# Optimization experiments

Hardware: AMD Instinct MI355X
Metric: run time of the kernel (lower is better)

## Reference

```python
import jax, jax.numpy as jnp
import numpy as np

B, S, A, H, NH = 4, 4096, 512, 1024, 16
HD = H // NH  # 64


def setup_inputs() -> dict:
    key = jax.random.key(0)
    ks = jax.random.split(key, 12)
    s = 1.0 / np.sqrt(H)
    return {
        "hidden_states": jax.random.normal(ks[0], (B, S, H), jnp.float32),
        "audio_tokens": jax.random.normal(ks[1], (B, A, H), jnp.float32),
        "attention_mask": jax.random.randint(ks[2], (B, A), 0, 2, jnp.int32),
        "Wq": jax.random.normal(ks[3], (H, H), jnp.float32) * s,
        "bq": jnp.zeros((H,), jnp.float32),
        "Wk": jax.random.normal(ks[4], (H, H), jnp.float32) * s,
        "bk": jnp.zeros((H,), jnp.float32),
        "Wv": jax.random.normal(ks[5], (H, H), jnp.float32) * s,
        "bv": jnp.zeros((H,), jnp.float32),
        "Wo": jax.random.normal(ks[6], (H, H), jnp.float32) * s,
        "bo": jnp.zeros((H,), jnp.float32),
        "ln_gamma": jnp.ones((H,), jnp.float32),
        "ln_beta": jnp.zeros((H,), jnp.float32),
        "residual_scale": jnp.asarray(0.05, jnp.float32),
    }


def _san(x, big=10000.0):
    return jnp.nan_to_num(x, nan=0.0, posinf=big, neginf=-big)


def reference(hidden_states, audio_tokens, attention_mask, Wq, bq, Wk, bk, Wv, bv,
              Wo, bo, ln_gamma, ln_beta, residual_scale):
    hs = _san(hidden_states).astype(jnp.float32)
    at = _san(audio_tokens).astype(jnp.float32)

    def heads(x, W, b):  # [b, t, H] -> [b, t, nh, hd]
        return _san(x @ W.T + b).reshape(x.shape[0], x.shape[1], NH, HD)

    q = heads(hs, Wq, bq)            # [B,S,NH,HD]
    k = heads(at, Wk, bk)            # [B,A,NH,HD]
    v = heads(at, Wv, bv)            # [B,A,NH,HD]

    scale = max(np.sqrt(HD), 1e-8)
    scores = jnp.einsum("bsnd,band->bnsa", q, k) / scale  # [B,NH,S,A]
    scores = jnp.clip(_san(jnp.clip(scores, -50.0, 50.0), 50.0), -50.0, 50.0)

    attend = (attention_mask > 0)[:, None, None, :]       # [B,1,1,A]
    scores = jnp.where(attend, scores, -10000.0)
    scores = jnp.clip(scores, -50.0, 50.0)

    probs = jax.nn.softmax(scores, axis=-1)
    probs = _san(probs, 1.0)
    probs = probs / (jnp.sum(probs, axis=-1, keepdims=True) + 1e-8)

    ctx = jnp.einsum("bnsa,band->bsnd", probs, v).reshape(B, S, H)
    delta = _san(ctx @ Wo.T + bo)

    rs = jnp.clip(residual_scale, 0.0, 0.3)
    delta = rs * delta

    mu = jnp.mean(delta, axis=-1, keepdims=True)
    var = jnp.mean(jnp.square(delta - mu), axis=-1, keepdims=True)
    delta = (delta - mu) / jnp.sqrt(var + 1e-5) * ln_gamma + ln_beta
    return delta
```

## Files before the change

### kernel.cpp

```cpp
#include <hip/hip_runtime.h>
#include <hip/hip_bf16.h>
#include <cstdint>
#include <cstddef>

#define B_  4
#define S_  4096
#define A_  512
#define H_  1024
#define NH_ 16
#define HD_ 64

typedef __bf16 bf16;
typedef __bf16 bf16x8 __attribute__((ext_vector_type(8)));
typedef __bf16 bf16x4 __attribute__((ext_vector_type(4)));
typedef float  fx4    __attribute__((ext_vector_type(4)));

typedef __attribute__((address_space(3))) void LDS_v;
typedef const __attribute__((address_space(1))) void GLB_v;

__device__ __forceinline__ void gl_lds16(const void* g, void* l) {
    __builtin_amdgcn_global_load_lds((GLB_v*)g, (LDS_v*)l, 16, 0, 0);
}

__device__ __forceinline__ float sanf(float x) {
    if (x != x) return 0.f;
    if (fabsf(x) == __builtin_inff()) return x > 0.f ? 10000.f : -10000.f;
    return x;
}

__global__ __launch_bounds__(256) void cast_all(const float* __restrict__ hs,
                                                const float* __restrict__ at,
                                                const float* __restrict__ wq,
                                                const float* __restrict__ wk,
                                                const float* __restrict__ wv,
                                                const float* __restrict__ wo,
                                                bf16* __restrict__ dhs, bf16* __restrict__ dat,
                                                bf16* __restrict__ dwq, bf16* __restrict__ dwk,
                                                bf16* __restrict__ dwv, bf16* __restrict__ dwo) {
    int i = blockIdx.x * 256 + threadIdx.x;
    const float* s; bf16* d; int off;
    if (i < 4194304)      { s = hs; d = dhs; off = i; }
    else if (i < 4718592) { s = at; d = dat; off = i - 4194304; }
    else if (i < 4980736) { s = wq; d = dwq; off = i - 4718592; }
    else if (i < 5242880) { s = wk; d = dwk; off = i - 4980736; }
    else if (i < 5505024) { s = wv; d = dwv; off = i - 5242880; }
    else                  { s = wo; d = dwo; off = i - 5505024; }
    float4 v = ((const float4*)s)[off];
    bf16x4 o;
    o[0] = (bf16)sanf(v.x); o[1] = (bf16)sanf(v.y);
    o[2] = (bf16)sanf(v.z); o[3] = (bf16)sanf(v.w);
    *(bf16x4*)&d[(size_t)off * 4] = o;
}

__global__ __launch_bounds__(256) void qkv_gemm(const bf16* __restrict__ hsb,
                                                const bf16* __restrict__ atb,
                                                const bf16* __restrict__ wqb,
                                                const bf16* __restrict__ wkb,
                                                const bf16* __restrict__ wvb,
                                                const float* __restrict__ bq,
                                                const float* __restrict__ bk,
                                                const float* __restrict__ bv,
                                                bf16* __restrict__ Qb,
                                                bf16* __restrict__ Kb,
                                                bf16* __restrict__ Vtb) {
    __shared__ __align__(16) bf16 As[128 * 32];
    __shared__ __align__(16) bf16 Bs[128 * 32];

    const int id = blockIdx.x;
    int mode, m0, n0;
    const bf16 *A, *Bt; const float* bias;
    if (id < 1024)      { mode = 0; m0 = (id & 127) * 128; n0 = (id >> 7) * 128; A = hsb; Bt = wqb; bias = bq; }
    else if (id < 1152) { int t = id - 1024; mode = 1; m0 = (t & 15) * 128; n0 = (t >> 4) * 128; A = atb; Bt = wkb; bias = bk; }
    else                { int t = id - 1152; mode = 2; m0 = (t & 15) * 128; n0 = (t >> 4) * 128; A = atb; Bt = wvb; bias = bv; }

    const int tid  = threadIdx.x;
    const int lane = tid & 63;
    const int wv   = tid >> 6;
    const int wr   = wv >> 1, wc = wv & 1;
    const int lr   = lane & 15, kq = lane >> 4;

    fx4 acc[4][4] = {};

    const bf16* Ag = A  + (size_t)m0 * 1024;
    const bf16* Bg = Bt + (size_t)n0 * 1024;
    const int c0 = tid, c1 = tid + 256;
    const int row0 = c0 >> 2, kc0 = c0 & 3;
    const int row1 = c1 >> 2, kc1 = c1 & 3;

    for (int k0 = 0; k0 < 1024; k0 += 32) {
        gl_lds16(Ag + (size_t)row0 * 1024 + k0 + kc0 * 8, &As[c0 * 8]);
        gl_lds16(Ag + (size_t)row1 * 1024 + k0 + kc1 * 8, &As[c1 * 8]);
        gl_lds16(Bg + (size_t)row0 * 1024 + k0 + kc0 * 8, &Bs[c0 * 8]);
        gl_lds16(Bg + (size_t)row1 * 1024 + k0 + kc1 * 8, &Bs[c1 * 8]);
        __syncthreads();
        bf16x8 af[4], bfr[4];
#pragma unroll
        for (int i = 0; i < 4; i++) af[i]  = *(const bf16x8*)&As[(wr * 64 + i * 16 + lr) * 32 + kq * 8];
#pragma unroll
        for (int j = 0; j < 4; j++) bfr[j] = *(const bf16x8*)&Bs[(wc * 64 + j * 16 + lr) * 32 + kq * 8];
#pragma unroll
        for (int i = 0; i < 4; i++)
#pragma unroll
            for (int j = 0; j < 4; j++)
                acc[i][j] = __builtin_amdgcn_mfma_f32_16x16x32_bf16(af[i], bfr[j], acc[i][j], 0, 0, 0);
        __syncthreads();
    }

    float bb[4];
#pragma unroll
    for (int j = 0; j < 4; j++) bb[j] = bias[n0 + wc * 64 + j * 16 + lr];

    if (mode == 0) {
        const float sc = 0.18033688011112042f;
#pragma unroll
        for (int i = 0; i < 4; i++) {
            int row = m0 + wr * 64 + i * 16 + kq * 4;
#pragma unroll
            for (int j = 0; j < 4; j++) {
                int col = n0 + wc * 64 + j * 16 + lr;
#pragma unroll
                for (int r = 0; r < 4; r++)
                    Qb[(size_t)(row + r) * 1024 + col] = (bf16)((acc[i][j][r] + bb[j]) * sc);
            }
        }
    } else if (mode == 1) {
#pragma unroll
        for (int i = 0; i < 4; i++) {
            int row = m0 + wr * 64 + i * 16 + kq * 4;
#pragma unroll
            for (int j = 0; j < 4; j++) {
                int col = n0 + wc * 64 + j * 16 + lr;
#pragma unroll
                for (int r = 0; r < 4; r++)
                    Kb[(size_t)(row + r) * 1024 + col] = (bf16)(acc[i][j][r] + bb[j]);
            }
        }
    } else {
#pragma unroll
        for (int i = 0; i < 4; i++) {
            int m = m0 + wr * 64 + i * 16 + kq * 4;
            int bidx = m >> 9, a = m & 511;
#pragma unroll
            for (int j = 0; j < 4; j++) {
                int col = n0 + wc * 64 + j * 16 + lr;
                bf16x4 o;
#pragma unroll
                for (int r = 0; r < 4; r++) o[r] = (bf16)(acc[i][j][r] + bb[j]);
                *(bf16x4*)&Vtb[((size_t)bidx * H_ + col) * A_ + a] = o;
            }
        }
    }
}

__global__ __launch_bounds__(256) void gemm_o(const bf16* __restrict__ A,
                                              const bf16* __restrict__ Bt,
                                              const float* __restrict__ bias,
                                              bf16* __restrict__ C,
                                              const float* __restrict__ rsp) {
    __shared__ __align__(16) bf16 As[128 * 32];
    __shared__ __align__(16) bf16 Bs[128 * 32];

    const int tid  = threadIdx.x;
    const int lane = tid & 63;
    const int wv   = tid >> 6;
    const int wr   = wv >> 1, wc = wv & 1;
    const int lr   = lane & 15, kq = lane >> 4;
    const int m0   = blockIdx.x * 128, n0 = blockIdx.y * 128;

    fx4 acc[4][4] = {};

    const bf16* Ag = A  + (size_t)m0 * 1024;
    const bf16* Bg = Bt + (size_t)n0 * 1024;
    const int c0 = tid, c1 = tid + 256;
    const int row0 = c0 >> 2, kc0 = c0 & 3;
    const int row1 = c1 >> 2, kc1 = c1 & 3;

    for (int k0 = 0; k0 < 1024; k0 += 32) {
        gl_lds16(Ag + (size_t)row0 * 1024 + k0 + kc0 * 8, &As[c0 * 8]);
        gl_lds16(Ag + (size_t)row1 * 1024 + k0 + kc1 * 8, &As[c1 * 8]);
        gl_lds16(Bg + (size_t)row0 * 1024 + k0 + kc0 * 8, &Bs[c0 * 8]);
        gl_lds16(Bg + (size_t)row1 * 1024 + k0 + kc1 * 8, &Bs[c1 * 8]);
        __syncthreads();
        bf16x8 af[4], bfr[4];
#pragma unroll
        for (int i = 0; i < 4; i++) af[i]  = *(const bf16x8*)&As[(wr * 64 + i * 16 + lr) * 32 + kq * 8];
#pragma unroll
        for (int j = 0; j < 4; j++) bfr[j] = *(const bf16x8*)&Bs[(wc * 64 + j * 16 + lr) * 32 + kq * 8];
#pragma unroll
        for (int i = 0; i < 4; i++)
#pragma unroll
            for (int j = 0; j < 4; j++)
                acc[i][j] = __builtin_amdgcn_mfma_f32_16x16x32_bf16(af[i], bfr[j], acc[i][j], 0, 0, 0);
        __syncthreads();
    }

    float bb[4];
#pragma unroll
    for (int j = 0; j < 4; j++) bb[j] = bias[n0 + wc * 64 + j * 16 + lr];
    float rs = fminf(fmaxf(rsp[0], 0.f), 0.3f);
#pragma unroll
    for (int i = 0; i < 4; i++) {
        int row = m0 + wr * 64 + i * 16 + kq * 4;
#pragma unroll
        for (int j = 0; j < 4; j++) {
            int col = n0 + wc * 64 + j * 16 + lr;
#pragma unroll
            for (int r = 0; r < 4; r++)
                C[(size_t)(row + r) * 1024 + col] = (bf16)(rs * (acc[i][j][r] + bb[j]));
        }
    }
}

__global__ __launch_bounds__(256, 4) void attn_kernel(const bf16* __restrict__ Q,
                                                      const bf16* __restrict__ Kb,
                                                      const bf16* __restrict__ Vt,
                                                      const int* __restrict__ mask,
                                                      bf16* __restrict__ ctx) {
    __shared__ __align__(16) bf16 Qs[128 * 72];
    __shared__ __align__(16) bf16 Ks[64 * 72];
    __shared__ __align__(16) bf16 Vts[64 * 72];
    __shared__ float smask[512];

    const int tid  = threadIdx.x;
    const int lane = tid & 63;
    const int wv   = tid >> 6;
    const int lr   = lane & 15, kq = lane >> 4;
    const int st = blockIdx.x, h = blockIdx.y, b = blockIdx.z;
    const int m0 = b * S_ + st * 128;
    const float LO = -72.134752f;

    bf16x8 qtmp[4];
#pragma unroll
    for (int i = 0; i < 4; i++) {
        int c = tid + i * 256, row = c >> 3, ch = c & 7;
        qtmp[i] = *(const bf16x8*)(Q + (size_t)(m0 + row) * H_ + h * 64 + ch * 8);
    }
    smask[tid]       = (mask[b * A_ + tid] > 0)       ? -LO : LO;
    smask[tid + 256] = (mask[b * A_ + tid + 256] > 0) ? -LO : LO;
#pragma unroll
    for (int i = 0; i < 4; i++) {
        int c = tid + i * 256, row = c >> 3, ch = c & 7;
        *(bf16x8*)&Qs[row * 72 + ch * 8] = qtmp[i];
    }

    const int srow = tid >> 2, sseg = tid & 3;
    const size_t kg = (size_t)(b * A_ + srow) * H_ + h * 64 + sseg * 16;
    const bf16* vrow = Vt + (size_t)(b * H_ + h * 64 + srow) * A_;
    const int va0 = 32 * (sseg >> 1) + 4 * ((2 * sseg) & 3);
    const int va1 = 32 * (sseg >> 1) + 4 * ((2 * sseg + 1) & 3);

    bf16x8 kr0 = *(const bf16x8*)(Kb + kg);
    bf16x8 kr1 = *(const bf16x8*)(Kb + kg + 8);
    bf16x4 v00 = *(const bf16x4*)(vrow + va0);
    bf16x4 v01 = *(const bf16x4*)(vrow + va0 + 16);
    bf16x4 v10 = *(const bf16x4*)(vrow + va1);
    bf16x4 v11 = *(const bf16x4*)(vrow + va1 + 16);

    fx4 acco[2][4] = {};
    fx4 accd[2] = {};

    bf16x8 vone;
#pragma unroll
    for (int e = 0; e < 8; e++) vone[e] = (bf16)1.0f;

    for (int it = 0; it < 8; it++) {
        const int a0 = it * 64;
        __syncthreads();
        *(bf16x8*)&Ks[srow * 72 + sseg * 16]      = kr0;
        *(bf16x8*)&Ks[srow * 72 + sseg * 16 + 8]  = kr1;
        *(bf16x8*)&Vts[srow * 72 + sseg * 16] =
            __builtin_shufflevector(v00, v01, 0, 1, 2, 3, 4, 5, 6, 7);
        *(bf16x8*)&Vts[srow * 72 + sseg * 16 + 8] =
            __builtin_shufflevector(v10, v11, 0, 1, 2, 3, 4, 5, 6, 7);
        __syncthreads();

        if (it < 7) {
            const size_t ko = kg + (size_t)(a0 + 64) * H_;
            kr0 = *(const bf16x8*)(Kb + ko);
            kr1 = *(const bf16x8*)(Kb + ko + 8);
            v00 = *(const bf16x4*)(vrow + a0 + 64 + va0);
            v01 = *(const bf16x4*)(vrow + a0 + 64 + va0 + 16);
            v10 = *(const bf16x4*)(vrow + a0 + 64 + va1);
            v11 = *(const bf16x4*)(vrow + a0 + 64 + va1 + 16);
        }

        fx4 accs[4][2] = {};
#pragma unroll
        for (int kk = 0; kk < 64; kk += 32) {
            bf16x8 kf[4], qf[2];
#pragma unroll
            for (int mt = 0; mt < 4; mt++)
                kf[mt] = *(const bf16x8*)&Ks[(mt * 16 + lr) * 72 + kk + kq * 8];
#pragma unroll
            for (int nt = 0; nt < 2; nt++)
                qf[nt] = *(const bf16x8*)&Qs[(wv * 32 + nt * 16 + lr) * 72 + kk + kq * 8];
#pragma unroll
            for (int mt = 0; mt < 4; mt++)
#pragma unroll
                for (int nt = 0; nt < 2; nt++)
                    accs[mt][nt] = __builtin_amdgcn_mfma_f32_16x16x32_bf16(kf[mt], qf[nt], accs[mt][nt], 0, 0, 0);
        }

        bf16x8 pa[2][2];
#pragma unroll
        for (int mt = 0; mt < 4; mt++) {
            fx4 cap = *(const fx4*)&smask[a0 + mt * 16 + kq * 4];
#pragma unroll
            for (int nt = 0; nt < 2; nt++) {
#pragma unroll
                for (int r = 0; r < 4; r++) {
                    float p = __builtin_amdgcn_exp2f(fminf(accs[mt][nt][r], cap[r]));
                    pa[mt >> 1][nt][(mt & 1) * 4 + r] = (bf16)p;
                }
            }
        }

#pragma unroll
        for (int ks = 0; ks < 2; ks++) {
#pragma unroll
            for (int stl = 0; stl < 2; stl++)
                accd[stl] = __builtin_amdgcn_mfma_f32_16x16x32_bf16(pa[ks][stl], vone, accd[stl], 0, 0, 0);
#pragma unroll
            for (int dt = 0; dt < 4; dt++) {
                bf16x8 vf = *(const bf16x8*)&Vts[(dt * 16 + lr) * 72 + ks * 32 + kq * 8];
#pragma unroll
                for (int stl = 0; stl < 2; stl++)
                    acco[stl][dt] = __builtin_amdgcn_mfma_f32_16x16x32_bf16(pa[ks][stl], vf, acco[stl][dt], 0, 0, 0);
            }
        }
    }

#pragma unroll
    for (int stl = 0; stl < 2; stl++) {
        float ri[4];
#pragma unroll
        for (int r = 0; r < 4; r++) ri[r] = __builtin_amdgcn_rcpf(accd[stl][r]);
#pragma unroll
        for (int dt = 0; dt < 4; dt++)
#pragma unroll
            for (int r = 0; r < 4; r++)
                Qs[(wv * 32 + stl * 16 + kq * 4 + r) * 72 + dt * 16 + lr] =
                    (bf16)(acco[stl][dt][r] * ri[r]);
    }
    __syncthreads();
#pragma unroll
    for (int i = 0; i < 4; i++) {
        int c = tid + i * 256, row = c >> 3, ch = c & 7;
        *(bf16x8*)&ctx[(size_t)(m0 + row) * H_ + h * 64 + ch * 8] = *(const bf16x8*)&Qs[row * 72 + ch * 8];
    }
}

__global__ __launch_bounds__(256) void ln_kernel(const bf16* __restrict__ in,
                                                 float* __restrict__ out,
                                                 const float* __restrict__ gamma,
                                                 const float* __restrict__ beta) {
    __shared__ float red[8];
    const int tid = threadIdx.x;
    bf16x4 xb = *(const bf16x4*)&in[(size_t)blockIdx.x * 1024 + tid * 4];
    float x0 = (float)xb[0], x1 = (float)xb[1], x2 = (float)xb[2], x3 = (float)xb[3];
    float s = x0 + x1 + x2 + x3;
    float q = x0 * x0 + x1 * x1 + x2 * x2 + x3 * x3;
#pragma unroll
    for (int off = 32; off > 0; off >>= 1) {
        s += __shfl_down(s, off);
        q += __shfl_down(q, off);
    }
    if ((tid & 63) == 0) { red[(tid >> 6) * 2] = s; red[(tid >> 6) * 2 + 1] = q; }
    __syncthreads();
    s = red[0] + red[2] + red[4] + red[6];
    q = red[1] + red[3] + red[5] + red[7];
    float mean = s * (1.f / 1024.f);
    float var  = q * (1.f / 1024.f) - mean * mean;
    float inv  = rsqrtf(var + 1e-5f);
    float4 g  = ((const float4*)gamma)[tid];
    float4 bb = ((const float4*)beta)[tid];
    float4 y;
    y.x = (x0 - mean) * inv * g.x + bb.x;
    y.y = (x1 - mean) * inv * g.y + bb.y;
    y.z = (x2 - mean) * inv * g.z + bb.z;
    y.w = (x3 - mean) * inv * g.w + bb.w;
    ((float4*)(out + (size_t)blockIdx.x * 1024))[tid] = y;
}

extern "C" void kernel_launch(void* const* d_in, const int* in_sizes, int n_in,
                              void* d_out, int out_size, void* d_ws, size_t ws_size,
                              hipStream_t stream) {
    const float* hs    = (const float*)d_in[0];
    const float* at    = (const float*)d_in[1];
    const int*   maskp = (const int*)d_in[2];
    const float* Wq    = (const float*)d_in[3];
    const float* bq    = (const float*)d_in[4];
    const float* Wk    = (const float*)d_in[5];
    const float* bk    = (const float*)d_in[6];
    const float* Wv    = (const float*)d_in[7];
    const float* bv    = (const float*)d_in[8];
    const float* Wo    = (const float*)d_in[9];
    const float* bo    = (const float*)d_in[10];
    const float* gamma = (const float*)d_in[11];
    const float* beta  = (const float*)d_in[12];
    const float* rsp   = (const float*)d_in[13];

    char* ws = (char*)d_ws;
    bf16* hsb = (bf16*)(ws + 0);
    bf16* ctx = (bf16*)(ws + 0);
    bf16* atb = (bf16*)(ws + 33554432);
    bf16* wqb = (bf16*)(ws + 37748736);
    bf16* wkb = (bf16*)(ws + 39845888);
    bf16* wvb = (bf16*)(ws + 41943040);
    bf16* wob = (bf16*)(ws + 44040192);
    bf16* Qb  = (bf16*)(ws + 46137344);
    bf16* Ob  = Qb;
    bf16* Kb  = (bf16*)(ws + 79691776);
    bf16* Vtb = (bf16*)(ws + 83886080);

    cast_all<<<22528, 256, 0, stream>>>(hs, at, Wq, Wk, Wv, Wo,
                                        hsb, atb, wqb, wkb, wvb, wob);

    qkv_gemm<<<1280, 256, 0, stream>>>(hsb, atb, wqb, wkb, wvb,
                                       bq, bk, bv, Qb, Kb, Vtb);

    attn_kernel<<<dim3(32, 16, 4), 256, 0, stream>>>(Qb, Kb, Vtb, maskp, ctx);

    gemm_o<<<dim3(128, 8), 256, 0, stream>>>(ctx, wob, bo, Ob, rsp);
    ln_kernel<<<16384, 256, 0, stream>>>(Ob, (float*)d_out, gamma, beta);
}
```

Measured before the change: 322.6 us.

## Use double-buffered 256x256 GEMM kernel for Q and output projections

Replaces the simple 128x128 single-buffered GEMMs used for the Q projection and the output projection with a new 512-thread 256x256-tile kernel. It double-buffers LDS, prefetches the next K slice during the MFMA phases, applies an XOR swizzle to LDS reads, raises wave priority around MFMA bursts and remaps block IDs for locality. The K/V projections are split into their own smaller kernel. The goal is to hide global-load latency and raise MFMA utilisation on the two large GEMMs. The cost is heavy register use from 8x4 accumulators per wave and only 256 blocks per launch, which may leave compute units underfilled.

```diff
diff --git a/kernel.cpp b/kernel.cpp
--- a/kernel.cpp
+++ b/kernel.cpp
@@ -52,26 +52,196 @@
     *(bf16x4*)&d[(size_t)off * 4] = o;
 }
 
-__global__ __launch_bounds__(256) void qkv_gemm(const bf16* __restrict__ hsb,
-                                                const bf16* __restrict__ atb,
-                                                const bf16* __restrict__ wqb,
-                                                const bf16* __restrict__ wkb,
-                                                const bf16* __restrict__ wvb,
-                                                const float* __restrict__ bq,
-                                                const float* __restrict__ bk,
-                                                const float* __restrict__ bv,
-                                                bf16* __restrict__ Qb,
-                                                bf16* __restrict__ Kb,
-                                                bf16* __restrict__ Vtb) {
+__global__ __launch_bounds__(512, 2) void gemm256(const bf16* __restrict__ A,
+                                                  const bf16* __restrict__ Bt,
+                                                  const float* __restrict__ bias,
+                                                  bf16* __restrict__ C,
+                                                  const int emode,
+                                                  const float* __restrict__ rsp) {
+    __shared__ __align__(16) bf16 lds[2][2][2][256][32];
+
+    const int tid  = threadIdx.x;
+    const int lane = tid & 63;
+    const int w8   = tid >> 6;
+    const int wm   = w8 >> 2, wn = w8 & 3;
+    const int lr   = lane & 15, kq = lane >> 4;
+    const int swz  = ((lr >> 3) & 1) << 4;
+
+    const int sid = ((blockIdx.x & 7) << 5) | (blockIdx.x >> 3);
+    const int m0 = (sid & 63) << 8, n0 = (sid >> 6) << 8;
+
+    const int g = lane ^ (((lane >> 5) & 1) << 1);
+    const bf16* Asrc = A  + (size_t)(m0 + w8 * 32 + (g >> 2)) * 1024 + (g & 3) * 8;
+    const bf16* Bsrc = Bt + (size_t)(n0 + w8 * 32 + (g >> 2)) * 1024 + (g & 3) * 8;
+
+#define STG(MS_, kh_, kt_, si_) do {                                                   \
+        const bf16* s_ = (MS_ ? Bsrc : Asrc) + (kt_) * 64 + (kh_) * 32;                \
+        gl_lds16(s_,                 &lds[si_][MS_][kh_][w8 * 32][0]      + lane * 8); \
+        gl_lds16(s_ + (size_t)16384, &lds[si_][MS_][kh_][w8 * 32 + 16][0] + lane * 8); \
+    } while (0)
+
+#define DSRA(i_, ks_, bi_) (*(const bf16x8*)(&lds[bi_][0][ks_][0][0] + \
+        ((((wm * 128 + (i_) * 16 + lr) * 32 + kq * 8)) ^ swz)))
+#define DSRB(j_, ks_, bi_) (*(const bf16x8*)(&lds[bi_][1][ks_][0][0] + \
+        ((((wn * 64 + (j_) * 16 + lr) * 32 + kq * 8)) ^ swz)))
+
+    fx4 acc[8][4] = {};
+
+    STG(0, 0, 0, 0); STG(1, 0, 0, 0); STG(0, 1, 0, 0); STG(1, 1, 0, 0);
+    asm volatile("s_waitcnt vmcnt(4)" ::: "memory");
+    __builtin_amdgcn_s_barrier();
+
+    for (int kt = 0; kt < 15; ++kt) {
+        const int bi = kt & 1, si = bi ^ 1, kn = kt + 1;
+        bf16x8 af[4], bfr[4];
+
+#pragma unroll
+        for (int j = 0; j < 4; j++) bfr[j] = DSRB(j, 0, bi);
+#pragma unroll
+        for (int i = 0; i < 4; i++) af[i] = DSRA(i, 0, bi);
+        STG(0, 0, kn, si);
+        __builtin_amdgcn_s_barrier();
+        asm volatile("s_waitcnt lgkmcnt(0)" ::: "memory");
+        __builtin_amdgcn_s_setprio(1);
+#pragma unroll
+        for (int i = 0; i < 4; i++)
+#pragma unroll
+            for (int j = 0; j < 4; j++)
+                acc[i][j] = __builtin_amdgcn_mfma_f32_16x16x32_bf16(af[i], bfr[j], acc[i][j], 0, 0, 0);
+        __builtin_amdgcn_s_setprio(0);
+        __builtin_amdgcn_s_barrier();
+
+#pragma unroll
+        for (int i = 0; i < 4; i++) af[i] = DSRA(i + 4, 0, bi);
+        STG(1, 0, kn, si);
+        __builtin_amdgcn_s_barrier();
+        asm volatile("s_waitcnt lgkmcnt(0)" ::: "memory");
+        __builtin_amdgcn_s_setprio(1);
+#pragma unroll
+        for (int i = 0; i < 4; i++)
+#pragma unroll
+            for (int j = 0; j < 4; j++)
+                acc[i + 4][j] = __builtin_amdgcn_mfma_f32_16x16x32_bf16(af[i], bfr[j], acc[i + 4][j], 0, 0, 0);
+        __builtin_amdgcn_s_setprio(0);
+        asm volatile("s_waitcnt vmcnt(4)" ::: "memory");
+        __builtin_amdgcn_s_barrier();
+
+#pragma unroll
+        for (int j = 0; j < 4; j++) bfr[j] = DSRB(j, 1, bi);
+#pragma unroll
+        for (int i = 0; i < 4; i++) af[i] = DSRA(i, 1, bi);
+        STG(0, 1, kn, si);
+        __builtin_amdgcn_s_barrier();
+        asm volatile("s_waitcnt lgkmcnt(0)" ::: "memory");
+        __builtin_amdgcn_s_setprio(1);
+#pragma unroll
+        for (int i = 0; i < 4; i++)
+#pragma unroll
+            for (int j = 0; j < 4; j++)
+                acc[i][j] = __builtin_amdgcn_mfma_f32_16x16x32_bf16(af[i], bfr[j], acc[i][j], 0, 0, 0);
+        __builtin_amdgcn_s_setprio(0);
+        __builtin_amdgcn_s_barrier();
+
+#pragma unroll
+        for (int i = 0; i < 4; i++) af[i] = DSRA(i + 4, 1, bi);
+        STG(1, 1, kn, si);
+        __builtin_amdgcn_s_barrier();
+        asm volatile("s_waitcnt lgkmcnt(0)" ::: "memory");
+        __builtin_amdgcn_s_setprio(1);
+#pragma unroll
+        for (int i = 0; i < 4; i++)
+#pragma unroll
+            for (int j = 0; j < 4; j++)
+                acc[i + 4][j] = __builtin_amdgcn_mfma_f32_16x16x32_bf16(af[i], bfr[j], acc[i + 4][j], 0, 0, 0);
+        __builtin_amdgcn_s_setprio(0);
+        asm volatile("s_waitcnt vmcnt(4)" ::: "memory");
+        __builtin_amdgcn_s_barrier();
+    }
+
+    {
+        const int bi = 1;
+        bf16x8 af[4], bfr[4];
+#pragma unroll
+        for (int j = 0; j < 4; j++) bfr[j] = DSRB(j, 0, bi);
+#pragma unroll
+        for (int i = 0; i < 4; i++) af[i] = DSRA(i, 0, bi);
+        __builtin_amdgcn_s_setprio(1);
+#pragma unroll
+        for (int i = 0; i < 4; i++)
+#pragma unroll
+            for (int j = 0; j < 4; j++)
+                acc[i][j] = __builtin_amdgcn_mfma_f32_16x16x32_bf16(af[i], bfr[j], acc[i][j], 0, 0, 0);
+        __builtin_amdgcn_s_setprio(0);
+#pragma unroll
+        for (int i = 0; i < 4; i++) af[i] = DSRA(i + 4, 0, bi);
+        __builtin_amdgcn_s_setprio(1);
+#pragma unroll
+        for (int i = 0; i < 4; i++)
+#pragma unroll
+            for (int j = 0; j < 4; j++)
+                acc[i + 4][j] = __builtin_amdgcn_mfma_f32_16x16x32_bf16(af[i], bfr[j], acc[i + 4][j], 0, 0, 0);
+        __builtin_amdgcn_s_setprio(0);
+        asm volatile("s_waitcnt vmcnt(0)" ::: "memory");
+        __builtin_amdgcn_s_barrier();
+#pragma unroll
+        for (int j = 0; j < 4; j++) bfr[j] = DSRB(j, 1, bi);
+#pragma unroll
+        for (int i = 0; i < 4; i++) af[i] = DSRA(i, 1, bi);
+        __builtin_amdgcn_s_setprio(1);
+#pragma unroll
+        for (int i = 0; i < 4; i++)
+#pragma unroll
+            for (int j = 0; j < 4; j++)
+                acc[i][j] = __builtin_amdgcn_mfma_f32_16x16x32_bf16(af[i], bfr[j], acc[i][j], 0, 0, 0);
+        __builtin_amdgcn_s_setprio(0);
+#pragma unroll
+        for (int i = 0; i < 4; i++) af[i] = DSRA(i + 4, 1, bi);
+        __builtin_amdgcn_s_setprio(1);
+#pragma unroll
+        for (int i = 0; i < 4; i++)
+#pragma unroll
+            for (int j = 0; j < 4; j++)
+                acc[i + 4][j] = __builtin_amdgcn_mfma_f32_16x16x32_bf16(af[i], bfr[j], acc[i + 4][j], 0, 0, 0);
+        __builtin_amdgcn_s_setprio(0);
+    }
+#undef STG
+#undef DSRA
+#undef DSRB
+
+    float bb[4];
+#pragma unroll
+    for (int j = 0; j < 4; j++) bb[j] = bias[n0 + wn * 64 + j * 16 + lr];
+    float sc;
+    if (emode == 0) sc = 0.18033688011112042f;
+    else            sc = fminf(fmaxf(rsp[0], 0.f), 0.3f);
+#pragma unroll
+    for (int i = 0; i < 8; i++) {
+        int row = m0 + wm * 128 + i * 16 + kq * 4;
+#pragma unroll
+        for (int j = 0; j < 4; j++) {
+            int col = n0 + wn * 64 + j * 16 + lr;
+#pragma unroll
+            for (int r = 0; r < 4; r++)
+                C[(size_t)(row + r) * 1024 + col] = (bf16)((acc[i][j][r] + bb[j]) * sc);
+        }
+    }
+}
+
+__global__ __launch_bounds__(256) void kv_gemm(const bf16* __restrict__ atb,
+                                               const bf16* __restrict__ wkb,
+                                               const bf16* __restrict__ wvb,
+                                               const float* __restrict__ bk,
+                                               const float* __restrict__ bv,
+                                               bf16* __restrict__ Kb,
+                                               bf16* __restrict__ Vtb) {
     __shared__ __align__(16) bf16 As[128 * 32];
     __shared__ __align__(16) bf16 Bs[128 * 32];
 
     const int id = blockIdx.x;
     int mode, m0, n0;
-    const bf16 *A, *Bt; const float* bias;
-    if (id < 1024)      { mode = 0; m0 = (id & 127) * 128; n0 = (id >> 7) * 128; A = hsb; Bt = wqb; bias = bq; }
-    else if (id < 1152) { int t = id - 1024; mode = 1; m0 = (t & 15) * 128; n0 = (t >> 4) * 128; A = atb; Bt = wkb; bias = bk; }
-    else                { int t = id - 1152; mode = 2; m0 = (t & 15) * 128; n0 = (t >> 4) * 128; A = atb; Bt = wvb; bias = bv; }
+    const bf16 *Bt; const float* bias;
+    if (id < 128) { mode = 1; m0 = (id & 15) * 128; n0 = (id >> 4) * 128; Bt = wkb; bias = bk; }
+    else          { int t = id - 128; mode = 2; m0 = (t & 15) * 128; n0 = (t >> 4) * 128; Bt = wvb; bias = bv; }
 
     const int tid  = threadIdx.x;
     const int lane = tid & 63;
@@ -81,8 +251,8 @@
 
     fx4 acc[4][4] = {};
 
-    const bf16* Ag = A  + (size_t)m0 * 1024;
-    const bf16* Bg = Bt + (size_t)n0 * 1024;
+    const bf16* Ag = atb + (size_t)m0 * 1024;
+    const bf16* Bg = Bt  + (size_t)n0 * 1024;
     const int c0 = tid, c1 = tid + 256;
     const int row0 = c0 >> 2, kc0 = c0 & 3;
     const int row1 = c1 >> 2, kc1 = c1 & 3;
@@ -110,20 +280,7 @@
 #pragma unroll
     for (int j = 0; j < 4; j++) bb[j] = bias[n0 + wc * 64 + j * 16 + lr];
 
-    if (mode == 0) {
-        const float sc = 0.18033688011112042f;
-#pragma unroll
-        for (int i = 0; i < 4; i++) {
-            int row = m0 + wr * 64 + i * 16 + kq * 4;
-#pragma unroll
-            for (int j = 0; j < 4; j++) {
-                int col = n0 + wc * 64 + j * 16 + lr;
-#pragma unroll
-                for (int r = 0; r < 4; r++)
-                    Qb[(size_t)(row + r) * 1024 + col] = (bf16)((acc[i][j][r] + bb[j]) * sc);
-            }
-        }
-    } else if (mode == 1) {
+    if (mode == 1) {
 #pragma unroll
         for (int i = 0; i < 4; i++) {
             int row = m0 + wr * 64 + i * 16 + kq * 4;
@@ -148,65 +305,6 @@
                 for (int r = 0; r < 4; r++) o[r] = (bf16)(acc[i][j][r] + bb[j]);
                 *(bf16x4*)&Vtb[((size_t)bidx * H_ + col) * A_ + a] = o;
             }
-        }
-    }
-}
-
-__global__ __launch_bounds__(256) void gemm_o(const bf16* __restrict__ A,
-                                              const bf16* __restrict__ Bt,
-                                              const float* __restrict__ bias,
-                                              bf16* __restrict__ C,
-                                              const float* __restrict__ rsp) {
-    __shared__ __align__(16) bf16 As[128 * 32];
-    __shared__ __align__(16) bf16 Bs[128 * 32];
-
-    const int tid  = threadIdx.x;
-    const int lane = tid & 63;
-    const int wv   = tid >> 6;
-    const int wr   = wv >> 1, wc = wv & 1;
-    const int lr   = lane & 15, kq = lane >> 4;
-    const int m0   = blockIdx.x * 128, n0 = blockIdx.y * 128;
-
-    fx4 acc[4][4] = {};
-
-    const bf16* Ag = A  + (size_t)m0 * 1024;
-    const bf16* Bg = Bt + (size_t)n0 * 1024;
-    const int c0 = tid, c1 = tid + 256;
-    const int row0 = c0 >> 2, kc0 = c0 & 3;
-    const int row1 = c1 >> 2, kc1 = c1 & 3;
-
-    for (int k0 = 0; k0 < 1024; k0 += 32) {
-        gl_lds16(Ag + (size_t)row0 * 1024 + k0 + kc0 * 8, &As[c0 * 8]);
-        gl_lds16(Ag + (size_t)row1 * 1024 + k0 + kc1 * 8, &As[c1 * 8]);
-        gl_lds16(Bg + (size_t)row0 * 1024 + k0 + kc0 * 8, &Bs[c0 * 8]);
-        gl_lds16(Bg + (size_t)row1 * 1024 + k0 + kc1 * 8, &Bs[c1 * 8]);
-        __syncthreads();
-        bf16x8 af[4], bfr[4];
-#pragma unroll
-        for (int i = 0; i < 4; i++) af[i]  = *(const bf16x8*)&As[(wr * 64 + i * 16 + lr) * 32 + kq * 8];
-#pragma unroll
-        for (int j = 0; j < 4; j++) bfr[j] = *(const bf16x8*)&Bs[(wc * 64 + j * 16 + lr) * 32 + kq * 8];
-#pragma unroll
-        for (int i = 0; i < 4; i++)
-#pragma unroll
-            for (int j = 0; j < 4; j++)
-                acc[i][j] = __builtin_amdgcn_mfma_f32_16x16x32_bf16(af[i], bfr[j], acc[i][j], 0, 0, 0);
-        __syncthreads();
-    }
-
-    float bb[4];
-#pragma unroll
-    for (int j = 0; j < 4; j++) bb[j] = bias[n0 + wc * 64 + j * 16 + lr];
-    float rs = fminf(fmaxf(rsp[0], 0.f), 0.3f);
-#pragma unroll
-    for (int i = 0; i < 4; i++) {
-        int row = m0 + wr * 64 + i * 16 + kq * 4;
-#pragma unroll
-        for (int j = 0; j < 4; j++) {
-            int col = n0 + wc * 64 + j * 16 + lr;
-#pragma unroll
-            for (int r = 0; r < 4; r++)
-                C[(size_t)(row + r) * 1024 + col] = (bf16)(rs * (acc[i][j][r] + bb[j]));
         }
     }
 }
@@ -416,11 +514,12 @@
     cast_all<<<22528, 256, 0, stream>>>(hs, at, Wq, Wk, Wv, Wo,
                                         hsb, atb, wqb, wkb, wvb, wob);
 
-    qkv_gemm<<<1280, 256, 0, stream>>>(hsb, atb, wqb, wkb, wvb,
-                                       bq, bk, bv, Qb, Kb, Vtb);
+    kv_gemm<<<256, 256, 0, stream>>>(atb, wkb, wvb, bk, bv, Kb, Vtb);
+
+    gemm256<<<256, 512, 0, stream>>>(hsb, wqb, bq, Qb, 0, rsp);
 
     attn_kernel<<<dim3(32, 16, 4), 256, 0, stream>>>(Qb, Kb, Vtb, maskp, ctx);
 
-    gemm_o<<<dim3(128, 8), 256, 0, stream>>>(ctx, wob, bo, Ob, rsp);
+    gemm256<<<256, 512, 0, stream>>>(ctx, wob, bo, Ob, 1, rsp);
     ln_kernel<<<16384, 256, 0, stream>>>(Ob, (float*)d_out, gamma, beta);
 }
```

Result: no change. 319.4 us (-1.0%).
